# Performance work log

Hardware: AMD Instinct MI355X
Metric: run time of the kernel (lower is better)

## Reference

```python
import jax, jax.numpy as jnp
import numpy as np


def _conv(x, w):
    # stride-2, pad-1, 3x3 conv, NCHW activations, HWIO kernel
    return jax.lax.conv_general_dilated(
        x, w, (2, 2), [(1, 1), (1, 1)],
        dimension_numbers=('NCHW', 'HWIO', 'NCHW'))


def setup_inputs() -> dict:
    key = jax.random.key(0)
    ks = iter(jax.random.split(key, 40))
    def rn(shape, scale=1.0):
        return jax.random.normal(next(ks), shape, jnp.float32) * scale
    d = {}
    d['img'] = rn((64, 3, 128, 128))
    d['qst'] = rn((64, 128))
    d['conv_w0'] = rn((3, 3, 3, 24), 1.0 / np.sqrt(3 * 9))
    for i in (1, 2, 3):
        d['conv_w%d' % i] = rn((3, 3, 24, 24), 1.0 / np.sqrt(24 * 9))
    for i in range(4):
        d['bn_s%d' % i] = jax.random.uniform(next(ks), (24,), jnp.float32, 0.5, 1.5)
        d['bn_b%d' % i] = rn((24,), 0.1)
    d['g_w1'] = rn((180, 256), 1.0 / np.sqrt(180))
    d['g_b1'] = rn((256,), 0.01)
    for i in (2, 3, 4):
        d['g_w%d' % i] = rn((256, 256), 1.0 / np.sqrt(256))
        d['g_b%d' % i] = rn((256,), 0.01)
    d['f_w1'] = rn((256, 256), 1.0 / np.sqrt(256))
    d['f_b1'] = rn((256,), 0.01)
    d['f_w2'] = rn((256, 256), 1.0 / np.sqrt(256))
    d['f_b2'] = rn((256,), 0.01)
    d['cls_w'] = rn((256, 32), 1.0 / np.sqrt(256))
    d['cls_b'] = rn((32,), 0.01)
    return d


def reference(img, qst, conv_w0, conv_w1, conv_w2, conv_w3,
              bn_s0, bn_b0, bn_s1, bn_b1, bn_s2, bn_b2, bn_s3, bn_b3,
              g_w1, g_b1, g_w2, g_b2, g_w3, g_b3, g_w4, g_b4,
              f_w1, f_b1, f_w2, f_b2, cls_w, cls_b):
    x = img
    for w, s, b in ((conv_w0, bn_s0, bn_b0), (conv_w1, bn_s1, bn_b1),
                    (conv_w2, bn_s2, bn_b2), (conv_w3, bn_s3, bn_b3)):
        x = jax.nn.relu(_conv(x, w) * s[None, :, None, None] + b[None, :, None, None])
    N, C, H, W = x.shape  # [64, 24, 8, 8]
    # positional encoding: coords_x, coords_y in [-1,1]
    cx, cy = jnp.meshgrid(jnp.linspace(-1.0, 1.0, W), jnp.linspace(-1.0, 1.0, H))
    pos = jnp.broadcast_to(jnp.stack([cx, cy])[None], (N, 2, H, W)).astype(x.dtype)
    x = jnp.concatenate([x, pos], axis=1)              # [N, C+2, H, W]
    Cf = C + 2
    x = x.transpose(0, 2, 3, 1).reshape(N, H * W, Cf)  # [N, HW, 26]
    # RN_G first linear decomposed over concat([x_i, x_j, qst]) so the huge
    # [N, HW, HW, 2C+q] concat tensor is never materialized (same math).
    W1a, W1b, W1c = g_w1[:Cf], g_w1[Cf:2 * Cf], g_w1[2 * Cf:]
    hi = x @ W1a                      # [N, HW, 256]
    hj = x @ W1b                      # [N, HW, 256]
    hq = qst @ W1c + g_b1             # [N, 256]
    h = jax.nn.relu(hi[:, :, None, :] + hj[:, None, :, :] + hq[:, None, None, :])  # [N,HW,HW,256]
    h = jax.nn.relu(h @ g_w2 + g_b2)
    h = jax.nn.relu(h @ g_w3 + g_b3)
    h = jax.nn.relu(h @ g_w4 + g_b4)
    s = h.sum(axis=(1, 2))            # sum over all HW*HW pairs -> [N, 256]
    # RN_F (dropout is identity in eval mode)
    y = jax.nn.relu(s @ f_w1 + f_b1)
    y = jax.nn.relu(y @ f_w2 + f_b2)
    return jax.nn.log_softmax(y @ cls_w + cls_b, axis=1)
```

## Files before the change

### kernel.cpp

```cpp
#include <hip/hip_runtime.h>
#include <hip/hip_bf16.h>
#include <math.h>

typedef __bf16 bf16x8 __attribute__((ext_vector_type(8)));
typedef __bf16 bf16x4 __attribute__((ext_vector_type(4)));
typedef float  f32x4  __attribute__((ext_vector_type(4)));

#define LH 264

__global__ __launch_bounds__(256) void conv0_k(const float* __restrict__ x, const float* __restrict__ w,
                                               const float* __restrict__ sc, const float* __restrict__ bi,
                                               float* __restrict__ y) {
  const int H = 128, W = 128, OH = 64, OW = 64;
  __shared__ float wl[9 * 3 * 24];
  for (int i = threadIdx.x; i < 9 * 3 * 24; i += 256) wl[i] = w[i];
  __syncthreads();

  int idx = blockIdx.x * 256 + threadIdx.x;
  int oxh = idx & 31; int t = idx >> 5; int oy = t & 63; int n = t >> 6;
  int ox0 = oxh * 2;

  float acc0[24], acc1[24];
#pragma unroll
  for (int co = 0; co < 24; ++co) { acc0[co] = 0.f; acc1[co] = 0.f; }

  for (int ci = 0; ci < 3; ++ci) {
    const float* xp = x + (size_t)(n * 3 + ci) * H * W;
#pragma unroll
    for (int ky = 0; ky < 3; ++ky) {
      int iy = 2 * oy + ky - 1;
      if (iy < 0 || iy >= H) continue;
      const float* row = xp + (size_t)iy * W;
      int ixb = 2 * ox0 - 1;
      float in[7];
#pragma unroll
      for (int u = 0; u < 7; ++u) {
        int ix = ixb + u;
        in[u] = (ix >= 0 && ix < W) ? row[ix] : 0.f;
      }
#pragma unroll
      for (int kx = 0; kx < 3; ++kx) {
        const float* wp = &wl[((ky * 3 + kx) * 3 + ci) * 24];
        float v0 = in[kx], v1 = in[kx + 2];
#pragma unroll
        for (int co = 0; co < 24; ++co) {
          float wv = wp[co];
          acc0[co] += v0 * wv;
          acc1[co] += v1 * wv;
        }
      }
    }
  }
  float* yp = y + (size_t)n * 24 * OH * OW + (size_t)oy * OW + ox0;
#pragma unroll
  for (int co = 0; co < 24; ++co) {
    float s = sc[co], b = bi[co];
    yp[(size_t)co * OH * OW]     = fmaxf(acc0[co] * s + b, 0.f);
    yp[(size_t)co * OH * OW + 1] = fmaxf(acc1[co] * s + b, 0.f);
  }
}

__global__ __launch_bounds__(256) void conv1_k(const float* __restrict__ x, const float* __restrict__ w,
                                               const float* __restrict__ sc, const float* __restrict__ bi,
                                               float* __restrict__ y) {
  const int H = 64, W = 64, OH = 32, OW = 32;
  __shared__ float wl[9 * 24 * 12];
  const int half = blockIdx.x & 1, sb = blockIdx.x >> 1;
  for (int i = threadIdx.x; i < 2592; i += 256) {
    int co = i % 12, rest = i / 12;
    wl[i] = w[rest * 24 + half * 12 + co];
  }
  __syncthreads();

  int idx = sb * 256 + threadIdx.x;
  int oxh = idx & 15; int tt = idx >> 4; int oy = tt & 31; int n = tt >> 5;
  int ox0 = oxh * 2;

  float acc0[12], acc1[12];
#pragma unroll
  for (int co = 0; co < 12; ++co) { acc0[co] = 0.f; acc1[co] = 0.f; }

  for (int ci = 0; ci < 24; ++ci) {
    const float* xp = x + (size_t)(n * 24 + ci) * H * W;
#pragma unroll
    for (int ky = 0; ky < 3; ++ky) {
      int iy = 2 * oy + ky - 1;
      if (iy < 0 || iy >= H) continue;
      const float* row = xp + (size_t)iy * W;
      int ixb = 2 * ox0 - 1;
      float in[7];
#pragma unroll
      for (int u = 0; u < 7; ++u) {
        int ix = ixb + u;
        in[u] = (ix >= 0 && ix < W) ? row[ix] : 0.f;
      }
#pragma unroll
      for (int kx = 0; kx < 3; ++kx) {
        const float* wp = &wl[((ky * 3 + kx) * 24 + ci) * 12];
        float v0 = in[kx], v1 = in[kx + 2];
#pragma unroll
        for (int co = 0; co < 12; ++co) {
          float wv = wp[co];
          acc0[co] += v0 * wv;
          acc1[co] += v1 * wv;
        }
      }
    }
  }
  float* yp = y + (size_t)n * 24 * OH * OW + (size_t)(half * 12) * OH * OW + (size_t)oy * OW + ox0;
#pragma unroll
  for (int co = 0; co < 12; ++co) {
    int cog = half * 12 + co;
    float s = sc[cog], b = bi[cog];
    yp[(size_t)co * OH * OW]     = fmaxf(acc0[co] * s + b, 0.f);
    yp[(size_t)co * OH * OW + 1] = fmaxf(acc1[co] * s + b, 0.f);
  }
}

__global__ __launch_bounds__(256) void mid_k(const float* __restrict__ c1,
    const float* __restrict__ w2, const float* __restrict__ bs2, const float* __restrict__ bb2,
    const float* __restrict__ gw1, const float* __restrict__ gb1, const float* __restrict__ qst,
    const float* __restrict__ g2, const float* __restrict__ g3, const float* __restrict__ g4,
    float* __restrict__ c2, float* __restrict__ hq, __bf16* __restrict__ Wt,
    float* __restrict__ sbuf) {
  __shared__ float smem[8224];
  const int blk = blockIdx.x, t = threadIdx.x;

  if (blk < 128) {
    const int half = blk & 1, sb = blk >> 1;
    for (int i = t; i < 2592; i += 256) {
      int co = i % 12, rest = i / 12;
      smem[i] = w2[rest * 24 + half * 12 + co];
    }
    __syncthreads();
    int idx = sb * 256 + t;
    int ox = idx & 15, oy = (idx >> 4) & 15, n = idx >> 8;
    const int H = 32, W = 32, OH = 16, OW = 16;
    float acc[12];
#pragma unroll
    for (int co = 0; co < 12; ++co) acc[co] = 0.f;
    for (int ci = 0; ci < 24; ++ci) {
      const float* xp = c1 + (size_t)(n * 24 + ci) * H * W;
#pragma unroll
      for (int ky = 0; ky < 3; ++ky) {
        int iy = 2 * oy + ky - 1;
        if (iy < 0 || iy >= H) continue;
#pragma unroll
        for (int kx = 0; kx < 3; ++kx) {
          int ix = 2 * ox + kx - 1;
          if (ix < 0 || ix >= W) continue;
          float v = xp[(size_t)iy * W + ix];
          const float* wp = &smem[((ky * 3 + kx) * 24 + ci) * 12];
#pragma unroll
          for (int co = 0; co < 12; ++co) acc[co] += v * wp[co];
        }
      }
    }
    float* yp = c2 + (size_t)n * 24 * OH * OW + (size_t)(half * 12) * OH * OW + (size_t)oy * OW + ox;
#pragma unroll
    for (int co = 0; co < 12; ++co) {
      int cog = half * 12 + co;
      yp[(size_t)co * OH * OW] = fmaxf(acc[co] * bs2[cog] + bb2[cog], 0.f);
    }

  } else if (blk < 152) {
    float* tile = smem;
    const int lb = blk - 128;
    const int l = lb >> 3, ks = lb & 7;
    const float* src = (l == 0) ? g2 : (l == 1) ? g3 : g4;
    for (int kk = 0; kk < 32; ++kk) tile[kk * 257 + t] = src[(ks * 32 + kk) * 256 + t];
    __syncthreads();
    const int q = t & 3, nb = t >> 2;
    __bf16* out = Wt + (size_t)(l * 8 + ks) * 8192;
#pragma unroll
    for (int i = 0; i < 4; ++i) {
      int nn = i * 64 + nb;
      bf16x8 v;
#pragma unroll
      for (int j = 0; j < 8; ++j) v[j] = (__bf16)tile[(q * 8 + j) * 257 + nn];
      *(bf16x8*)&out[nn * 32 + q * 8] = v;
    }

  } else {
    const int n = blk - 152;
    sbuf[n * 256 + t] = 0.f;
    float* qs = smem;
    if (t < 128) qs[t] = qst[n * 128 + t];
    __syncthreads();
    float a = gb1[t];
    for (int c = 0; c < 128; ++c) a += qs[c] * gw1[(52 + c) * 256 + t];
    hq[n * 256 + t] = a;
  }
}

__global__ __launch_bounds__(256) void tail_k(const float* __restrict__ c2,
    const float* __restrict__ w3, const float* __restrict__ bs3, const float* __restrict__ bb3,
    const float* __restrict__ gw1, float* __restrict__ hi, float* __restrict__ hj) {
  __shared__ float w3l[5184];
  __shared__ float cs2[6144];
  __shared__ float s3[1536];
  const int n = blockIdx.x, t = threadIdx.x;
  for (int i = t; i < 5184; i += 256) w3l[i] = w3[i];
  for (int i = t; i < 6144; i += 256) cs2[i] = c2[(size_t)n * 6144 + i];
  __syncthreads();

  const int pos = t & 63, cog = t >> 6;
  const int oy = pos >> 3, ox = pos & 7;
  float acc[6];
#pragma unroll
  for (int u = 0; u < 6; ++u) acc[u] = 0.f;
  for (int ci = 0; ci < 24; ++ci) {
    const float* cp = &cs2[ci * 256];
#pragma unroll
    for (int ky = 0; ky < 3; ++ky) {
      int iy = 2 * oy + ky - 1;
      if (iy < 0 || iy >= 16) continue;
#pragma unroll
      for (int kx = 0; kx < 3; ++kx) {
        int ix = 2 * ox + kx - 1;
        if (ix < 0 || ix >= 16) continue;
        float v = cp[iy * 16 + ix];
        const float* wp = &w3l[((ky * 3 + kx) * 24 + ci) * 24 + cog * 6];
#pragma unroll
        for (int u = 0; u < 6; ++u) acc[u] += v * wp[u];
      }
    }
  }
#pragma unroll
  for (int u = 0; u < 6; ++u) {
    int co = cog * 6 + u;
    s3[co * 64 + pos] = fmaxf(acc[u] * bs3[co] + bb3[co], 0.f);
  }

  float wa[26], wb[26];
#pragma unroll
  for (int c = 0; c < 26; ++c) {
    wa[c] = gw1[c * 256 + t];
    wb[c] = gw1[(26 + c) * 256 + t];
  }
  __syncthreads();
  for (int p = 0; p < 64; ++p) {
    float a = 0.f, b = 0.f;
#pragma unroll
    for (int c = 0; c < 24; ++c) {
      float v = s3[c * 64 + p];
      a += v * wa[c];
      b += v * wb[c];
    }
    float cx = -1.f + (2.f / 7.f) * (float)(p & 7);
    float cy = -1.f + (2.f / 7.f) * (float)(p >> 3);
    a += cx * wa[24] + cy * wa[25];
    b += cx * wb[24] + cy * wb[25];
    hi[(size_t)(n * 64 + p) * 256 + t] = a;
    hj[(size_t)(n * 64 + p) * 256 + t] = b;
  }
}

__global__ __launch_bounds__(256, 2)
void g_fused(const float* __restrict__ hi, const float* __restrict__ hj,
             const float* __restrict__ hq, const __bf16* __restrict__ Wt,
             const float* __restrict__ b2, const float* __restrict__ b3,
             const float* __restrict__ b4, float* __restrict__ s_out) {
  const int blk = blockIdx.x;
  const int n = blk >> 5, ib = blk & 31;
  const int tid = threadIdx.x;
  const int wave = tid >> 6, lane = tid & 63;
  const int q = lane >> 4, lr = lane & 15;

  __shared__ __align__(16) __bf16 Hs[128 * LH];

  const int c0 = (tid & 63) * 4;
  float4 hq4 = *(const float4*)(hq + (size_t)n * 256 + c0);
  float4 h0 = *(const float4*)(hi + (size_t)(n * 64 + ib * 2)     * 256 + c0);
  float4 h1 = *(const float4*)(hi + (size_t)(n * 64 + ib * 2 + 1) * 256 + c0);
  h0.x += hq4.x; h0.y += hq4.y; h0.z += hq4.z; h0.w += hq4.w;
  h1.x += hq4.x; h1.y += hq4.y; h1.z += hq4.z; h1.w += hq4.w;

  const float* hjb = hj + (size_t)n * 64 * 256;
#pragma unroll
  for (int it = 0; it < 16; ++it) {
    int j = it * 4 + wave;
    float4 v = *(const float4*)(hjb + j * 256 + c0);
    bf16x4 o;
    o[0] = (__bf16)fmaxf(v.x + h0.x, 0.f);
    o[1] = (__bf16)fmaxf(v.y + h0.y, 0.f);
    o[2] = (__bf16)fmaxf(v.z + h0.z, 0.f);
    o[3] = (__bf16)fmaxf(v.w + h0.w, 0.f);
    *(bf16x4*)&Hs[j * LH + c0] = o;
    bf16x4 o2;
    o2[0] = (__bf16)fmaxf(v.x + h1.x, 0.f);
    o2[1] = (__bf16)fmaxf(v.y + h1.y, 0.f);
    o2[2] = (__bf16)fmaxf(v.z + h1.z, 0.f);
    o2[3] = (__bf16)fmaxf(v.w + h1.w, 0.f);
    *(bf16x4*)&Hs[(64 + j) * LH + c0] = o2;
  }
  __syncthreads();

  const int colloc = wave * 64 + lr;
  const __bf16* Bp = Wt + (size_t)wave * 2048 + lr * 32 + q * 8;

  for (int l = 0; l < 3; ++l) {
    const __bf16* Bl = Bp + (size_t)l * 65536;
    const float* bl = (l == 0) ? b2 : (l == 1) ? b3 : b4;

    f32x4 acc[8][4];
#pragma unroll
    for (int r = 0; r < 8; ++r)
#pragma unroll
      for (int c = 0; c < 4; ++c) acc[r][c] = (f32x4){0.f, 0.f, 0.f, 0.f};

    for (int ks = 0; ks < 8; ++ks) {
      bf16x8 b[4];
#pragma unroll
      for (int c = 0; c < 4; ++c)
        b[c] = *(const bf16x8*)&Bl[ks * 8192 + c * 512];
      bf16x8 a[8];
#pragma unroll
      for (int r = 0; r < 8; ++r)
        a[r] = *(const bf16x8*)&Hs[(r * 16 + lr) * LH + ks * 32 + q * 8];
#pragma unroll
      for (int r = 0; r < 8; ++r)
#pragma unroll
        for (int c = 0; c < 4; ++c)
          acc[r][c] = __builtin_amdgcn_mfma_f32_16x16x32_bf16(a[r], b[c], acc[r][c], 0, 0, 0);
    }

    float bias[4];
#pragma unroll
    for (int c = 0; c < 4; ++c) bias[c] = bl[colloc + c * 16];

    if (l < 2) {
      __syncthreads();
#pragma unroll
      for (int r = 0; r < 8; ++r)
#pragma unroll
        for (int c = 0; c < 4; ++c)
#pragma unroll
          for (int reg = 0; reg < 4; ++reg) {
            int row = r * 16 + q * 4 + reg;
            Hs[row * LH + colloc + c * 16] = (__bf16)fmaxf(acc[r][c][reg] + bias[c], 0.f);
          }
      __syncthreads();
    } else {
#pragma unroll
      for (int c = 0; c < 4; ++c) {
        float cs = 0.f;
#pragma unroll
        for (int r = 0; r < 8; ++r)
#pragma unroll
          for (int reg = 0; reg < 4; ++reg)
            cs += fmaxf(acc[r][c][reg] + bias[c], 0.f);
        cs += __shfl_xor(cs, 16);
        cs += __shfl_xor(cs, 32);
        if (q == 0) atomicAdd(&s_out[n * 256 + colloc + c * 16], cs);
      }
    }
  }
}

__global__ void f_net(const float* __restrict__ s, const float* __restrict__ fw1,
                      const float* __restrict__ fb1, const float* __restrict__ fw2,
                      const float* __restrict__ fb2, const float* __restrict__ cw,
                      const float* __restrict__ cb, float* __restrict__ out) {
  int n = blockIdx.x, t = threadIdx.x;
  __shared__ float buf[256], buf2[256], zs[32];
  buf[t] = s[n * 256 + t];
  __syncthreads();
  float a = fb1[t];
  for (int c = 0; c < 256; ++c) a += buf[c] * fw1[c * 256 + t];
  a = fmaxf(a, 0.f);
  buf2[t] = a;
  __syncthreads();
  float y = fb2[t];
  for (int c = 0; c < 256; ++c) y += buf2[c] * fw2[c * 256 + t];
  y = fmaxf(y, 0.f);
  __syncthreads();
  buf[t] = y;
  __syncthreads();
  float z = 0.f;
  if (t < 32) {
    z = cb[t];
    for (int c = 0; c < 256; ++c) z += buf[c] * cw[c * 32 + t];
    zs[t] = z;
  }
  __syncthreads();
  if (t < 32) {
    float m = -1e30f;
    for (int c = 0; c < 32; ++c) m = fmaxf(m, zs[c]);
    float se = 0.f;
    for (int c = 0; c < 32; ++c) se += expf(zs[c] - m);
    out[n * 32 + t] = z - m - logf(se);
  }
}

extern "C" void kernel_launch(void* const* d_in, const int* in_sizes, int n_in,
                              void* d_out, int out_size, void* d_ws, size_t ws_size,
                              hipStream_t stream) {
  const float* img  = (const float*)d_in[0];
  const float* qst  = (const float*)d_in[1];
  const float* w0   = (const float*)d_in[2];
  const float* w1   = (const float*)d_in[3];
  const float* w2   = (const float*)d_in[4];
  const float* w3   = (const float*)d_in[5];
  const float* bs0  = (const float*)d_in[6];
  const float* bb0  = (const float*)d_in[7];
  const float* bs1  = (const float*)d_in[8];
  const float* bb1  = (const float*)d_in[9];
  const float* bs2  = (const float*)d_in[10];
  const float* bb2  = (const float*)d_in[11];
  const float* bs3  = (const float*)d_in[12];
  const float* bb3  = (const float*)d_in[13];
  const float* gw1  = (const float*)d_in[14];
  const float* gb1  = (const float*)d_in[15];
  const float* gw2  = (const float*)d_in[16];
  const float* gb2  = (const float*)d_in[17];
  const float* gw3  = (const float*)d_in[18];
  const float* gb3  = (const float*)d_in[19];
  const float* gw4  = (const float*)d_in[20];
  const float* gb4  = (const float*)d_in[21];
  const float* fw1  = (const float*)d_in[22];
  const float* fb1  = (const float*)d_in[23];
  const float* fw2  = (const float*)d_in[24];
  const float* fb2  = (const float*)d_in[25];
  const float* cw   = (const float*)d_in[26];
  const float* cb   = (const float*)d_in[27];

  char* ws = (char*)d_ws;
  float* c0 = (float*)(ws + 0);
  float* c1 = (float*)(ws + 25165824);
  float* c2 = (float*)(ws + 31457280);
  float*  hi  = (float*)(ws + 0);
  float*  hj  = (float*)(ws + 4194304);
  float*  hqb = (float*)(ws + 8388608);
  float*  sbuf = (float*)(ws + 8454144);
  __bf16* Wt  = (__bf16*)(ws + 8519680);

  conv0_k<<<512, 256, 0, stream>>>(img, w0, bs0, bb0, c0);
  conv1_k<<<256, 256, 0, stream>>>(c0, w1, bs1, bb1, c1);
  mid_k<<<216, 256, 0, stream>>>(c1, w2, bs2, bb2, gw1, gb1, qst, gw2, gw3, gw4,
                                 c2, hqb, Wt, sbuf);
  tail_k<<<64, 256, 0, stream>>>(c2, w3, bs3, bb3, gw1, hi, hj);
  g_fused<<<2048, 256, 0, stream>>>(hi, hj, hqb, Wt, gb2, gb3, gb4, sbuf);
  f_net<<<64, 256, 0, stream>>>(sbuf, fw1, fb1, fw2, fb2, cw, cb, (float*)d_out);
}
```

Baseline: 316.7 us.

## Fuse all stages into one cooperative persistent kernel with grid syncs

Replaces the six separate kernel launches with one cooperative persistent kernel that loops over work items per phase, separated by grid-wide syncs, with the old multi-kernel path kept as a fallback. Stages are regrouped: conv1 runs alongside the weight transpose and the qst projection, and conv2+conv3+hi/hj are fused per image so the c2 tensor stays in shared memory. The g_fused LDS tile drops row padding in favour of an XOR-like rotation swizzle. The goal is to remove launch gaps and a global round-trip. The cost is that the grid is capped by occupancy (65KB LDS per block), so heavy phases like conv0 and g_fused run with fewer concurrent blocks, and grid.sync adds its own overhead.

```diff
diff --git a/kernel.cpp b/kernel.cpp
--- a/kernel.cpp
+++ b/kernel.cpp
@@ -1,31 +1,37 @@
 #include <hip/hip_runtime.h>
 #include <hip/hip_bf16.h>
+#include <hip/hip_cooperative_groups.h>
 #include <math.h>
+
+namespace cg = cooperative_groups;
 
 typedef __bf16 bf16x8 __attribute__((ext_vector_type(8)));
 typedef __bf16 bf16x4 __attribute__((ext_vector_type(4)));
 typedef float  f32x4  __attribute__((ext_vector_type(4)));
 
-#define LH 264
-
-__global__ __launch_bounds__(256) void conv0_k(const float* __restrict__ x, const float* __restrict__ w,
-                                               const float* __restrict__ sc, const float* __restrict__ bi,
-                                               float* __restrict__ y) {
+struct Ctx {
+  const float *img, *qst;
+  const float *w0, *bs0, *bb0, *w1, *bs1, *bb1, *w2, *bs2, *bb2, *w3, *bs3, *bb3;
+  const float *gw1, *gb1, *g2, *g3, *g4, *gb2, *gb3, *gb4;
+  const float *fw1, *fb1, *fw2, *fb2, *cw, *cb;
+  float *c0, *c1, *hi, *hj, *hq, *sbuf, *out;
+  __bf16 *Wt;
+};
+
+
+__device__ __forceinline__ void ph_conv0(const Ctx& A, int w, int t, float* smem) {
+  float* wl = smem;
+  for (int i = t; i < 648; i += 256) wl[i] = A.w0[i];
+  __syncthreads();
   const int H = 128, W = 128, OH = 64, OW = 64;
-  __shared__ float wl[9 * 3 * 24];
-  for (int i = threadIdx.x; i < 9 * 3 * 24; i += 256) wl[i] = w[i];
-  __syncthreads();
-
-  int idx = blockIdx.x * 256 + threadIdx.x;
-  int oxh = idx & 31; int t = idx >> 5; int oy = t & 63; int n = t >> 6;
+  int idx = w * 256 + t;
+  int oxh = idx & 31; int tt = idx >> 5; int oy = tt & 63; int n = tt >> 6;
   int ox0 = oxh * 2;
-
   float acc0[24], acc1[24];
 #pragma unroll
   for (int co = 0; co < 24; ++co) { acc0[co] = 0.f; acc1[co] = 0.f; }
-
   for (int ci = 0; ci < 3; ++ci) {
-    const float* xp = x + (size_t)(n * 3 + ci) * H * W;
+    const float* xp = A.img + (size_t)(n * 3 + ci) * H * W;
 #pragma unroll
     for (int ky = 0; ky < 3; ++ky) {
       int iy = 2 * oy + ky - 1;
@@ -51,127 +57,76 @@
       }
     }
   }
-  float* yp = y + (size_t)n * 24 * OH * OW + (size_t)oy * OW + ox0;
+  float* yp = A.c0 + (size_t)n * 24 * OH * OW + (size_t)oy * OW + ox0;
 #pragma unroll
   for (int co = 0; co < 24; ++co) {
-    float s = sc[co], b = bi[co];
+    float s = A.bs0[co], b = A.bb0[co];
     yp[(size_t)co * OH * OW]     = fmaxf(acc0[co] * s + b, 0.f);
     yp[(size_t)co * OH * OW + 1] = fmaxf(acc1[co] * s + b, 0.f);
   }
 }
 
-__global__ __launch_bounds__(256) void conv1_k(const float* __restrict__ x, const float* __restrict__ w,
-                                               const float* __restrict__ sc, const float* __restrict__ bi,
-                                               float* __restrict__ y) {
-  const int H = 64, W = 64, OH = 32, OW = 32;
-  __shared__ float wl[9 * 24 * 12];
-  const int half = blockIdx.x & 1, sb = blockIdx.x >> 1;
-  for (int i = threadIdx.x; i < 2592; i += 256) {
-    int co = i % 12, rest = i / 12;
-    wl[i] = w[rest * 24 + half * 12 + co];
-  }
-  __syncthreads();
-
-  int idx = sb * 256 + threadIdx.x;
-  int oxh = idx & 15; int tt = idx >> 4; int oy = tt & 31; int n = tt >> 5;
-  int ox0 = oxh * 2;
-
-  float acc0[12], acc1[12];
-#pragma unroll
-  for (int co = 0; co < 12; ++co) { acc0[co] = 0.f; acc1[co] = 0.f; }
-
-  for (int ci = 0; ci < 24; ++ci) {
-    const float* xp = x + (size_t)(n * 24 + ci) * H * W;
-#pragma unroll
-    for (int ky = 0; ky < 3; ++ky) {
-      int iy = 2 * oy + ky - 1;
-      if (iy < 0 || iy >= H) continue;
-      const float* row = xp + (size_t)iy * W;
-      int ixb = 2 * ox0 - 1;
-      float in[7];
-#pragma unroll
-      for (int u = 0; u < 7; ++u) {
-        int ix = ixb + u;
-        in[u] = (ix >= 0 && ix < W) ? row[ix] : 0.f;
-      }
-#pragma unroll
-      for (int kx = 0; kx < 3; ++kx) {
-        const float* wp = &wl[((ky * 3 + kx) * 24 + ci) * 12];
-        float v0 = in[kx], v1 = in[kx + 2];
-#pragma unroll
-        for (int co = 0; co < 12; ++co) {
-          float wv = wp[co];
-          acc0[co] += v0 * wv;
-          acc1[co] += v1 * wv;
-        }
-      }
-    }
-  }
-  float* yp = y + (size_t)n * 24 * OH * OW + (size_t)(half * 12) * OH * OW + (size_t)oy * OW + ox0;
-#pragma unroll
-  for (int co = 0; co < 12; ++co) {
-    int cog = half * 12 + co;
-    float s = sc[cog], b = bi[cog];
-    yp[(size_t)co * OH * OW]     = fmaxf(acc0[co] * s + b, 0.f);
-    yp[(size_t)co * OH * OW + 1] = fmaxf(acc1[co] * s + b, 0.f);
-  }
-}
-
-__global__ __launch_bounds__(256) void mid_k(const float* __restrict__ c1,
-    const float* __restrict__ w2, const float* __restrict__ bs2, const float* __restrict__ bb2,
-    const float* __restrict__ gw1, const float* __restrict__ gb1, const float* __restrict__ qst,
-    const float* __restrict__ g2, const float* __restrict__ g3, const float* __restrict__ g4,
-    float* __restrict__ c2, float* __restrict__ hq, __bf16* __restrict__ Wt,
-    float* __restrict__ sbuf) {
-  __shared__ float smem[8224];
-  const int blk = blockIdx.x, t = threadIdx.x;
-
-  if (blk < 128) {
-    const int half = blk & 1, sb = blk >> 1;
+__device__ __forceinline__ void ph_role1(const Ctx& A, int w, int t, char* smraw) {
+  float* smem = (float*)smraw;
+  if (w < 256) {
+    float* wl = smem;
+    const int half = w & 1, sb = w >> 1;
     for (int i = t; i < 2592; i += 256) {
       int co = i % 12, rest = i / 12;
-      smem[i] = w2[rest * 24 + half * 12 + co];
+      wl[i] = A.w1[rest * 24 + half * 12 + co];
     }
     __syncthreads();
+    const int H = 64, W = 64, OH = 32, OW = 32;
     int idx = sb * 256 + t;
-    int ox = idx & 15, oy = (idx >> 4) & 15, n = idx >> 8;
-    const int H = 32, W = 32, OH = 16, OW = 16;
-    float acc[12];
-#pragma unroll
-    for (int co = 0; co < 12; ++co) acc[co] = 0.f;
+    int oxh = idx & 15; int tt = idx >> 4; int oy = tt & 31; int n = tt >> 5;
+    int ox0 = oxh * 2;
+    float acc0[12], acc1[12];
+#pragma unroll
+    for (int co = 0; co < 12; ++co) { acc0[co] = 0.f; acc1[co] = 0.f; }
     for (int ci = 0; ci < 24; ++ci) {
-      const float* xp = c1 + (size_t)(n * 24 + ci) * H * W;
+      const float* xp = A.c0 + (size_t)(n * 24 + ci) * H * W;
 #pragma unroll
       for (int ky = 0; ky < 3; ++ky) {
         int iy = 2 * oy + ky - 1;
         if (iy < 0 || iy >= H) continue;
+        const float* row = xp + (size_t)iy * W;
+        int ixb = 2 * ox0 - 1;
+        float in[7];
+#pragma unroll
+        for (int u = 0; u < 7; ++u) {
+          int ix = ixb + u;
+          in[u] = (ix >= 0 && ix < W) ? row[ix] : 0.f;
+        }
 #pragma unroll
         for (int kx = 0; kx < 3; ++kx) {
-          int ix = 2 * ox + kx - 1;
-          if (ix < 0 || ix >= W) continue;
-          float v = xp[(size_t)iy * W + ix];
-          const float* wp = &smem[((ky * 3 + kx) * 24 + ci) * 12];
-#pragma unroll
-          for (int co = 0; co < 12; ++co) acc[co] += v * wp[co];
+          const float* wp = &wl[((ky * 3 + kx) * 24 + ci) * 12];
+          float v0 = in[kx], v1 = in[kx + 2];
+#pragma unroll
+          for (int co = 0; co < 12; ++co) {
+            float wv = wp[co];
+            acc0[co] += v0 * wv;
+            acc1[co] += v1 * wv;
+          }
         }
       }
     }
-    float* yp = c2 + (size_t)n * 24 * OH * OW + (size_t)(half * 12) * OH * OW + (size_t)oy * OW + ox;
+    float* yp = A.c1 + (size_t)n * 24 * OH * OW + (size_t)(half * 12) * OH * OW + (size_t)oy * OW + ox0;
 #pragma unroll
     for (int co = 0; co < 12; ++co) {
       int cog = half * 12 + co;
-      yp[(size_t)co * OH * OW] = fmaxf(acc[co] * bs2[cog] + bb2[cog], 0.f);
-    }
-
-  } else if (blk < 152) {
+      float s = A.bs1[cog], b = A.bb1[cog];
+      yp[(size_t)co * OH * OW]     = fmaxf(acc0[co] * s + b, 0.f);
+      yp[(size_t)co * OH * OW + 1] = fmaxf(acc1[co] * s + b, 0.f);
+    }
+  } else if (w < 280) {
     float* tile = smem;
-    const int lb = blk - 128;
+    const int lb = w - 256;
     const int l = lb >> 3, ks = lb & 7;
-    const float* src = (l == 0) ? g2 : (l == 1) ? g3 : g4;
+    const float* src = (l == 0) ? A.g2 : (l == 1) ? A.g3 : A.g4;
     for (int kk = 0; kk < 32; ++kk) tile[kk * 257 + t] = src[(ks * 32 + kk) * 256 + t];
     __syncthreads();
     const int q = t & 3, nb = t >> 2;
-    __bf16* out = Wt + (size_t)(l * 8 + ks) * 8192;
+    __bf16* out = A.Wt + (size_t)(l * 8 + ks) * 8192;
 #pragma unroll
     for (int i = 0; i < 4; ++i) {
       int nn = i * 64 + nb;
@@ -180,63 +135,88 @@
       for (int j = 0; j < 8; ++j) v[j] = (__bf16)tile[(q * 8 + j) * 257 + nn];
       *(bf16x8*)&out[nn * 32 + q * 8] = v;
     }
-
   } else {
-    const int n = blk - 152;
-    sbuf[n * 256 + t] = 0.f;
     float* qs = smem;
-    if (t < 128) qs[t] = qst[n * 128 + t];
+    const int n = w - 280;
+    A.sbuf[n * 256 + t] = 0.f;
+    if (t < 128) qs[t] = A.qst[n * 128 + t];
     __syncthreads();
-    float a = gb1[t];
-    for (int c = 0; c < 128; ++c) a += qs[c] * gw1[(52 + c) * 256 + t];
-    hq[n * 256 + t] = a;
-  }
-}
-
-__global__ __launch_bounds__(256) void tail_k(const float* __restrict__ c2,
-    const float* __restrict__ w3, const float* __restrict__ bs3, const float* __restrict__ bb3,
-    const float* __restrict__ gw1, float* __restrict__ hi, float* __restrict__ hj) {
-  __shared__ float w3l[5184];
-  __shared__ float cs2[6144];
-  __shared__ float s3[1536];
-  const int n = blockIdx.x, t = threadIdx.x;
-  for (int i = t; i < 5184; i += 256) w3l[i] = w3[i];
-  for (int i = t; i < 6144; i += 256) cs2[i] = c2[(size_t)n * 6144 + i];
-  __syncthreads();
-
-  const int pos = t & 63, cog = t >> 6;
-  const int oy = pos >> 3, ox = pos & 7;
-  float acc[6];
-#pragma unroll
-  for (int u = 0; u < 6; ++u) acc[u] = 0.f;
-  for (int ci = 0; ci < 24; ++ci) {
-    const float* cp = &cs2[ci * 256];
-#pragma unroll
-    for (int ky = 0; ky < 3; ++ky) {
-      int iy = 2 * oy + ky - 1;
-      if (iy < 0 || iy >= 16) continue;
-#pragma unroll
-      for (int kx = 0; kx < 3; ++kx) {
-        int ix = 2 * ox + kx - 1;
-        if (ix < 0 || ix >= 16) continue;
-        float v = cp[iy * 16 + ix];
-        const float* wp = &w3l[((ky * 3 + kx) * 24 + ci) * 24 + cog * 6];
-#pragma unroll
-        for (int u = 0; u < 6; ++u) acc[u] += v * wp[u];
-      }
-    }
-  }
-#pragma unroll
-  for (int u = 0; u < 6; ++u) {
-    int co = cog * 6 + u;
-    s3[co * 64 + pos] = fmaxf(acc[u] * bs3[co] + bb3[co], 0.f);
-  }
-
+    float a = A.gb1[t];
+    for (int c = 0; c < 128; ++c) a += qs[c] * A.gw1[(52 + c) * 256 + t];
+    A.hq[n * 256 + t] = a;
+  }
+}
+
+__device__ __forceinline__ void ph_chain2(const Ctx& A, int w, int t, float* smem) {
+  float* sw = smem;
+  float* s2 = smem + 5184;
+  float* s3 = smem + 11328;
+  const int n = w;
+  for (int i = t; i < 5184; i += 256) sw[i] = A.w2[i];
+  __syncthreads();
+  {
+    int ox = t & 15, oy = t >> 4;
+    float acc[24];
+#pragma unroll
+    for (int co = 0; co < 24; ++co) acc[co] = 0.f;
+    for (int ci = 0; ci < 24; ++ci) {
+      const float* xp = A.c1 + (size_t)(n * 24 + ci) * 1024;
+#pragma unroll
+      for (int ky = 0; ky < 3; ++ky) {
+        int iy = 2 * oy + ky - 1;
+        if (iy < 0 || iy >= 32) continue;
+#pragma unroll
+        for (int kx = 0; kx < 3; ++kx) {
+          int ix = 2 * ox + kx - 1;
+          if (ix < 0 || ix >= 32) continue;
+          float v = xp[iy * 32 + ix];
+          const float* wp = &sw[((ky * 3 + kx) * 24 + ci) * 24];
+#pragma unroll
+          for (int co = 0; co < 24; ++co) acc[co] += v * wp[co];
+        }
+      }
+    }
+#pragma unroll
+    for (int co = 0; co < 24; ++co)
+      s2[co * 256 + t] = fmaxf(acc[co] * A.bs2[co] + A.bb2[co], 0.f);
+  }
+  __syncthreads();
+  for (int i = t; i < 5184; i += 256) sw[i] = A.w3[i];
+  __syncthreads();
+  {
+    const int pos = t & 63, cog = t >> 6;
+    const int oy = pos >> 3, ox = pos & 7;
+    float acc[6];
+#pragma unroll
+    for (int u = 0; u < 6; ++u) acc[u] = 0.f;
+    for (int ci = 0; ci < 24; ++ci) {
+      const float* cp = &s2[ci * 256];
+#pragma unroll
+      for (int ky = 0; ky < 3; ++ky) {
+        int iy = 2 * oy + ky - 1;
+        if (iy < 0 || iy >= 16) continue;
+#pragma unroll
+        for (int kx = 0; kx < 3; ++kx) {
+          int ix = 2 * ox + kx - 1;
+          if (ix < 0 || ix >= 16) continue;
+          float v = cp[iy * 16 + ix];
+          const float* wp = &sw[((ky * 3 + kx) * 24 + ci) * 24 + cog * 6];
+#pragma unroll
+          for (int u = 0; u < 6; ++u) acc[u] += v * wp[u];
+        }
+      }
+    }
+#pragma unroll
+    for (int u = 0; u < 6; ++u) {
+      int co = cog * 6 + u;
+      s3[co * 64 + pos] = fmaxf(acc[u] * A.bs3[co] + A.bb3[co], 0.f);
+    }
+  }
   float wa[26], wb[26];
 #pragma unroll
   for (int c = 0; c < 26; ++c) {
-    wa[c] = gw1[c * 256 + t];
-    wb[c] = gw1[(26 + c) * 256 + t];
+    wa[c] = A.gw1[c * 256 + t];
+    wb[c] = A.gw1[(26 + c) * 256 + t];
   }
   __syncthreads();
   for (int p = 0; p < 64; ++p) {
@@ -251,57 +231,52 @@
     float cy = -1.f + (2.f / 7.f) * (float)(p >> 3);
     a += cx * wa[24] + cy * wa[25];
     b += cx * wb[24] + cy * wb[25];
-    hi[(size_t)(n * 64 + p) * 256 + t] = a;
-    hj[(size_t)(n * 64 + p) * 256 + t] = b;
-  }
-}
-
-__global__ __launch_bounds__(256, 2)
-void g_fused(const float* __restrict__ hi, const float* __restrict__ hj,
-             const float* __restrict__ hq, const __bf16* __restrict__ Wt,
-             const float* __restrict__ b2, const float* __restrict__ b3,
-             const float* __restrict__ b4, float* __restrict__ s_out) {
-  const int blk = blockIdx.x;
+    A.hi[(size_t)(n * 64 + p) * 256 + t] = a;
+    A.hj[(size_t)(n * 64 + p) * 256 + t] = b;
+  }
+}
+
+__device__ __forceinline__ void ph_gfused(const Ctx& A, int blk, int tid, char* smraw) {
+  __bf16* Hs = (__bf16*)smraw;
   const int n = blk >> 5, ib = blk & 31;
-  const int tid = threadIdx.x;
   const int wave = tid >> 6, lane = tid & 63;
   const int q = lane >> 4, lr = lane & 15;
-
-  __shared__ __align__(16) __bf16 Hs[128 * LH];
-
   const int c0 = (tid & 63) * 4;
-  float4 hq4 = *(const float4*)(hq + (size_t)n * 256 + c0);
-  float4 h0 = *(const float4*)(hi + (size_t)(n * 64 + ib * 2)     * 256 + c0);
-  float4 h1 = *(const float4*)(hi + (size_t)(n * 64 + ib * 2 + 1) * 256 + c0);
+
+  float4 hq4 = *(const float4*)(A.hq + (size_t)n * 256 + c0);
+  float4 h0 = *(const float4*)(A.hi + (size_t)(n * 64 + ib * 2)     * 256 + c0);
+  float4 h1 = *(const float4*)(A.hi + (size_t)(n * 64 + ib * 2 + 1) * 256 + c0);
   h0.x += hq4.x; h0.y += hq4.y; h0.z += hq4.z; h0.w += hq4.w;
   h1.x += hq4.x; h1.y += hq4.y; h1.z += hq4.z; h1.w += hq4.w;
 
-  const float* hjb = hj + (size_t)n * 64 * 256;
+  const float* hjb = A.hj + (size_t)n * 64 * 256;
 #pragma unroll
   for (int it = 0; it < 16; ++it) {
     int j = it * 4 + wave;
     float4 v = *(const float4*)(hjb + j * 256 + c0);
+    int rc = (c0 + ((j & 7) << 4)) & 255;
     bf16x4 o;
     o[0] = (__bf16)fmaxf(v.x + h0.x, 0.f);
     o[1] = (__bf16)fmaxf(v.y + h0.y, 0.f);
     o[2] = (__bf16)fmaxf(v.z + h0.z, 0.f);
     o[3] = (__bf16)fmaxf(v.w + h0.w, 0.f);
-    *(bf16x4*)&Hs[j * LH + c0] = o;
+    *(bf16x4*)&Hs[j * 256 + rc] = o;
     bf16x4 o2;
     o2[0] = (__bf16)fmaxf(v.x + h1.x, 0.f);
     o2[1] = (__bf16)fmaxf(v.y + h1.y, 0.f);
     o2[2] = (__bf16)fmaxf(v.z + h1.z, 0.f);
     o2[3] = (__bf16)fmaxf(v.w + h1.w, 0.f);
-    *(bf16x4*)&Hs[(64 + j) * LH + c0] = o2;
+    *(bf16x4*)&Hs[(64 + j) * 256 + rc] = o2;
   }
   __syncthreads();
 
   const int colloc = wave * 64 + lr;
-  const __bf16* Bp = Wt + (size_t)wave * 2048 + lr * 32 + q * 8;
+  const __bf16* Bp = A.Wt + (size_t)wave * 2048 + lr * 32 + q * 8;
+  const int arot = (lr & 7) << 4;
 
   for (int l = 0; l < 3; ++l) {
     const __bf16* Bl = Bp + (size_t)l * 65536;
-    const float* bl = (l == 0) ? b2 : (l == 1) ? b3 : b4;
+    const float* bl = (l == 0) ? A.gb2 : (l == 1) ? A.gb3 : A.gb4;
 
     f32x4 acc[8][4];
 #pragma unroll
@@ -310,6 +285,7 @@
       for (int c = 0; c < 4; ++c) acc[r][c] = (f32x4){0.f, 0.f, 0.f, 0.f};
 
     for (int ks = 0; ks < 8; ++ks) {
+      int astart = (ks * 32 + q * 8 + arot) & 255;
       bf16x8 b[4];
 #pragma unroll
       for (int c = 0; c < 4; ++c)
@@ -317,7 +293,7 @@
       bf16x8 a[8];
 #pragma unroll
       for (int r = 0; r < 8; ++r)
-        a[r] = *(const bf16x8*)&Hs[(r * 16 + lr) * LH + ks * 32 + q * 8];
+        a[r] = *(const bf16x8*)&Hs[(r * 16 + lr) * 256 + astart];
 #pragma unroll
       for (int r = 0; r < 8; ++r)
 #pragma unroll
@@ -338,7 +314,8 @@
 #pragma unroll
           for (int reg = 0; reg < 4; ++reg) {
             int row = r * 16 + q * 4 + reg;
-            Hs[row * LH + colloc + c * 16] = (__bf16)fmaxf(acc[r][c][reg] + bias[c], 0.f);
+            int wc = (colloc + c * 16 + ((row & 7) << 4)) & 255;
+            Hs[row * 256 + wc] = (__bf16)fmaxf(acc[r][c][reg] + bias[c], 0.f);
           }
       __syncthreads();
     } else {
@@ -352,35 +329,34 @@
             cs += fmaxf(acc[r][c][reg] + bias[c], 0.f);
         cs += __shfl_xor(cs, 16);
         cs += __shfl_xor(cs, 32);
-        if (q == 0) atomicAdd(&s_out[n * 256 + colloc + c * 16], cs);
-      }
-    }
-  }
-}
-
-__global__ void f_net(const float* __restrict__ s, const float* __restrict__ fw1,
-                      const float* __restrict__ fb1, const float* __restrict__ fw2,
-                      const float* __restrict__ fb2, const float* __restrict__ cw,
-                      const float* __restrict__ cb, float* __restrict__ out) {
-  int n = blockIdx.x, t = threadIdx.x;
-  __shared__ float buf[256], buf2[256], zs[32];
-  buf[t] = s[n * 256 + t];
-  __syncthreads();
-  float a = fb1[t];
-  for (int c = 0; c < 256; ++c) a += buf[c] * fw1[c * 256 + t];
+        if (q == 0) atomicAdd(&A.sbuf[n * 256 + colloc + c * 16], cs);
+      }
+    }
+  }
+}
+
+__device__ __forceinline__ void ph_fnet(const Ctx& A, int w, int t, float* smem) {
+  float* buf  = smem;
+  float* buf2 = smem + 256;
+  float* zs   = smem + 512;
+  const int n = w;
+  buf[t] = A.sbuf[n * 256 + t];
+  __syncthreads();
+  float a = A.fb1[t];
+  for (int c = 0; c < 256; ++c) a += buf[c] * A.fw1[c * 256 + t];
   a = fmaxf(a, 0.f);
   buf2[t] = a;
   __syncthreads();
-  float y = fb2[t];
-  for (int c = 0; c < 256; ++c) y += buf2[c] * fw2[c * 256 + t];
+  float y = A.fb2[t];
+  for (int c = 0; c < 256; ++c) y += buf2[c] * A.fw2[c * 256 + t];
   y = fmaxf(y, 0.f);
   __syncthreads();
   buf[t] = y;
   __syncthreads();
   float z = 0.f;
   if (t < 32) {
-    z = cb[t];
-    for (int c = 0; c < 256; ++c) z += buf[c] * cw[c * 32 + t];
+    z = A.cb[t];
+    for (int c = 0; c < 256; ++c) z += buf[c] * A.cw[c * 32 + t];
     zs[t] = z;
   }
   __syncthreads();
@@ -389,57 +365,94 @@
     for (int c = 0; c < 32; ++c) m = fmaxf(m, zs[c]);
     float se = 0.f;
     for (int c = 0; c < 32; ++c) se += expf(zs[c] - m);
-    out[n * 32 + t] = z - m - logf(se);
-  }
+    A.out[n * 32 + t] = z - m - logf(se);
+  }
+}
+
+__global__ __launch_bounds__(256, 2) void mega(Ctx A) {
+  cg::grid_group grid = cg::this_grid();
+  __shared__ __align__(16) char sm[65536];
+  const int t = threadIdx.x;
+  const int G = gridDim.x;
+  for (int w = blockIdx.x; w < 512; w += G)  { __syncthreads(); ph_conv0(A, w, t, (float*)sm); }
+  grid.sync();
+  for (int w = blockIdx.x; w < 344; w += G)  { __syncthreads(); ph_role1(A, w, t, sm); }
+  grid.sync();
+  for (int w = blockIdx.x; w < 64; w += G)   { __syncthreads(); ph_chain2(A, w, t, (float*)sm); }
+  grid.sync();
+  for (int w = blockIdx.x; w < 2048; w += G) { __syncthreads(); ph_gfused(A, w, t, sm); }
+  grid.sync();
+  for (int w = blockIdx.x; w < 64; w += G)   { __syncthreads(); ph_fnet(A, w, t, (float*)sm); }
+}
+
+__global__ __launch_bounds__(256) void k_conv0(Ctx A) {
+  __shared__ float sm[648];
+  ph_conv0(A, blockIdx.x, threadIdx.x, sm);
+}
+__global__ __launch_bounds__(256) void k_role1(Ctx A) {
+  __shared__ __align__(16) char sm[32896];
+  ph_role1(A, blockIdx.x, threadIdx.x, sm);
+}
+__global__ __launch_bounds__(256) void k_chain2(Ctx A) {
+  __shared__ float sm[12864];
+  ph_chain2(A, blockIdx.x, threadIdx.x, sm);
+}
+__global__ __launch_bounds__(256, 2) void k_gfused(Ctx A) {
+  __shared__ __align__(16) char sm[65536];
+  ph_gfused(A, blockIdx.x, threadIdx.x, sm);
+}
+__global__ __launch_bounds__(256) void k_fnet(Ctx A) {
+  __shared__ float sm[544];
+  ph_fnet(A, blockIdx.x, threadIdx.x, sm);
 }
 
 extern "C" void kernel_launch(void* const* d_in, const int* in_sizes, int n_in,
                               void* d_out, int out_size, void* d_ws, size_t ws_size,
                               hipStream_t stream) {
-  const float* img  = (const float*)d_in[0];
-  const float* qst  = (const float*)d_in[1];
-  const float* w0   = (const float*)d_in[2];
-  const float* w1   = (const float*)d_in[3];
-  const float* w2   = (const float*)d_in[4];
-  const float* w3   = (const float*)d_in[5];
-  const float* bs0  = (const float*)d_in[6];
-  const float* bb0  = (const float*)d_in[7];
-  const float* bs1  = (const float*)d_in[8];
-  const float* bb1  = (const float*)d_in[9];
-  const float* bs2  = (const float*)d_in[10];
-  const float* bb2  = (const float*)d_in[11];
-  const float* bs3  = (const float*)d_in[12];
-  const float* bb3  = (const float*)d_in[13];
-  const float* gw1  = (const float*)d_in[14];
-  const float* gb1  = (const float*)d_in[15];
-  const float* gw2  = (const float*)d_in[16];
-  const float* gb2  = (const float*)d_in[17];
-  const float* gw3  = (const float*)d_in[18];
-  const float* gb3  = (const float*)d_in[19];
-  const float* gw4  = (const float*)d_in[20];
-  const float* gb4  = (const float*)d_in[21];
-  const float* fw1  = (const float*)d_in[22];
-  const float* fb1  = (const float*)d_in[23];
-  const float* fw2  = (const float*)d_in[24];
-  const float* fb2  = (const float*)d_in[25];
-  const float* cw   = (const float*)d_in[26];
-  const float* cb   = (const float*)d_in[27];
-
   char* ws = (char*)d_ws;
   float* c0 = (float*)(ws + 0);
   float* c1 = (float*)(ws + 25165824);
-  float* c2 = (float*)(ws + 31457280);
+  __bf16* Wt  = (__bf16*)(ws + 31457280);
+  float*  hqb = (float*)(ws + 31850496);
+  float*  sbuf = (float*)(ws + 31916032);
   float*  hi  = (float*)(ws + 0);
   float*  hj  = (float*)(ws + 4194304);
-  float*  hqb = (float*)(ws + 8388608);
-  float*  sbuf = (float*)(ws + 8454144);
-  __bf16* Wt  = (__bf16*)(ws + 8519680);
-
-  conv0_k<<<512, 256, 0, stream>>>(img, w0, bs0, bb0, c0);
-  conv1_k<<<256, 256, 0, stream>>>(c0, w1, bs1, bb1, c1);
-  mid_k<<<216, 256, 0, stream>>>(c1, w2, bs2, bb2, gw1, gb1, qst, gw2, gw3, gw4,
-                                 c2, hqb, Wt, sbuf);
-  tail_k<<<64, 256, 0, stream>>>(c2, w3, bs3, bb3, gw1, hi, hj);
-  g_fused<<<2048, 256, 0, stream>>>(hi, hj, hqb, Wt, gb2, gb3, gb4, sbuf);
-  f_net<<<64, 256, 0, stream>>>(sbuf, fw1, fb1, fw2, fb2, cw, cb, (float*)d_out);
-}
+
+  Ctx A;
+  A.img = (const float*)d_in[0];  A.qst = (const float*)d_in[1];
+  A.w0  = (const float*)d_in[2];  A.bs0 = (const float*)d_in[6];  A.bb0 = (const float*)d_in[7];
+  A.w1  = (const float*)d_in[3];  A.bs1 = (const float*)d_in[8];  A.bb1 = (const float*)d_in[9];
+  A.w2  = (const float*)d_in[4];  A.bs2 = (const float*)d_in[10]; A.bb2 = (const float*)d_in[11];
+  A.w3  = (const float*)d_in[5];  A.bs3 = (const float*)d_in[12]; A.bb3 = (const float*)d_in[13];
+  A.gw1 = (const float*)d_in[14]; A.gb1 = (const float*)d_in[15];
+  A.g2  = (const float*)d_in[16]; A.gb2 = (const float*)d_in[17];
+  A.g3  = (const float*)d_in[18]; A.gb3 = (const float*)d_in[19];
+  A.g4  = (const float*)d_in[20]; A.gb4 = (const float*)d_in[21];
+  A.fw1 = (const float*)d_in[22]; A.fb1 = (const float*)d_in[23];
+  A.fw2 = (const float*)d_in[24]; A.fb2 = (const float*)d_in[25];
+  A.cw  = (const float*)d_in[26]; A.cb  = (const float*)d_in[27];
+  A.c0 = c0; A.c1 = c1; A.hi = hi; A.hj = hj; A.hq = hqb; A.sbuf = sbuf;
+  A.Wt = Wt; A.out = (float*)d_out;
+
+  int dev = 0;
+  hipGetDevice(&dev);
+  int coopSupported = 0;
+  hipDeviceGetAttribute(&coopSupported, hipDeviceAttributeCooperativeLaunch, dev);
+  int numCU = 0;
+  hipDeviceGetAttribute(&numCU, hipDeviceAttributeMultiprocessorCount, dev);
+  int nb = 0;
+  hipError_t qe = hipOccupancyMaxActiveBlocksPerMultiprocessor(&nb, (const void*)mega, 256, 0);
+  long long maxg = (qe == hipSuccess && numCU > 0) ? (long long)nb * numCU : 0;
+
+  if (coopSupported && maxg >= 64) {
+    int grid = (int)(maxg < 512 ? maxg : 512);
+    void* params[] = { &A };
+    hipLaunchCooperativeKernel((const void*)mega, dim3(grid), dim3(256), params, 0, stream);
+  } else {
+    k_conv0<<<512, 256, 0, stream>>>(A);
+    k_role1<<<344, 256, 0, stream>>>(A);
+    k_chain2<<<64, 256, 0, stream>>>(A);
+    k_gfused<<<2048, 256, 0, stream>>>(A);
+    k_fnet<<<64, 256, 0, stream>>>(A);
+  }
+}
```

After: 542.4 us. +71.3%, slower.
